# Optimization experiments

Measured on AMD Instinct MI355X. Metric: run time of the kernel, lower is better.

The kernel has to match this reference:

```python
import jax, jax.numpy as jnp
import numpy as np

HEADS = 4
NEG_SLOPE = 0.2  # PyG GATConv default


def gat_layer(x, src, dst, W, a_src, a_dst, b):
    """PyG-style GATConv: gather -> per-edge attention -> segment softmax -> scatter.
    x: [N, Fin], W: [Fin, H*C], a_src/a_dst: [H, C], b: [H*C]."""
    N = x.shape[0]
    h = (x @ W).reshape(N, HEADS, -1)                      # [N, H, C]
    alpha_s = jnp.einsum('nhc,hc->nh', h, a_src)           # [N, H]
    alpha_d = jnp.einsum('nhc,hc->nh', h, a_dst)           # [N, H]
    e = jax.nn.leaky_relu(alpha_s[src] + alpha_d[dst], NEG_SLOPE)  # [E, H]
    # segment softmax over incoming edges of each destination node
    m = jax.ops.segment_max(e, dst, num_segments=N)
    m = jnp.where(jnp.isfinite(m), m, 0.0)
    ex = jnp.exp(e - m[dst])
    denom = jax.ops.segment_sum(ex, dst, num_segments=N)
    alpha = ex / (denom[dst] + 1e-16)                      # [E, H]
    msg = h[src] * alpha[:, :, None]                       # [E, H, C]
    out = jax.ops.segment_sum(msg, dst, num_segments=N)    # [N, H, C]
    return out.reshape(N, -1) + b


def setup_inputs() -> dict:
    key = jax.random.key(0)
    ks = jax.random.split(key, 10)
    N, E, FIN, HID, OUT = 50000, 800000, 128, 128, 128
    hd1, hd2 = HID // HEADS, OUT // HEADS
    x = jax.random.normal(ks[0], (N, FIN), dtype=jnp.float32)
    edge_index = jax.random.randint(ks[1], (2, E), 0, N, dtype=jnp.int32)
    s1 = 1.0 / np.sqrt(FIN)
    s2 = 1.0 / np.sqrt(HID)
    return {
        'x_sub': x,
        'edge_index_sub': edge_index,
        'W1': jax.random.normal(ks[2], (FIN, HEADS * hd1), dtype=jnp.float32) * s1,
        'a_src1': jax.random.normal(ks[3], (HEADS, hd1), dtype=jnp.float32) * 0.1,
        'a_dst1': jax.random.normal(ks[4], (HEADS, hd1), dtype=jnp.float32) * 0.1,
        'b1': jnp.zeros((HEADS * hd1,), dtype=jnp.float32),
        'W2': jax.random.normal(ks[5], (HID, HEADS * hd2), dtype=jnp.float32) * s2,
        'a_src2': jax.random.normal(ks[6], (HEADS, hd2), dtype=jnp.float32) * 0.1,
        'a_dst2': jax.random.normal(ks[7], (HEADS, hd2), dtype=jnp.float32) * 0.1,
        'b2': jnp.zeros((HEADS * hd2,), dtype=jnp.float32),
    }


def reference(x_sub, edge_index_sub, W1, a_src1, a_dst1, b1, W2, a_src2, a_dst2, b2):
    N = x_sub.shape[0]
    # PyG GATConv default add_self_loops=True
    loops = jnp.arange(N, dtype=edge_index_sub.dtype)
    src = jnp.concatenate([edge_index_sub[0], loops])
    dst = jnp.concatenate([edge_index_sub[1], loops])
    h = gat_layer(x_sub, src, dst, W1, a_src1, a_dst1, b1)
    h = jax.nn.relu(h)  # dropout p=0.5 is identity in eval mode
    out = gat_layer(h, src, dst, W2, a_src2, a_dst2, b2)
    return out
```

## Files before the change

kernel.cpp:

```cpp
#include <hip/hip_runtime.h>
#include <hip/hip_fp16.h>

#define HEADS 4
#define F 128
#define NEG_SLOPE 0.2f

#define NB 256
#define NPB 196
#define BE 8192
#define CAPS 6144

#define LDP 136

typedef _Float16 f16x8 __attribute__((ext_vector_type(8)));
typedef _Float16 f16x4 __attribute__((ext_vector_type(4)));
typedef float f32x4 __attribute__((ext_vector_type(4)));

__device__ __forceinline__ float lrelu(float v) { return v > 0.f ? v : NEG_SLOPE * v; }

__global__ __launch_bounds__(256) void k_wcvt_hist(const float* __restrict__ W1,
                                                   const float* __restrict__ W2,
                                                   _Float16* __restrict__ Wt1,
                                                   _Float16* __restrict__ Wt2,
                                                   const int* __restrict__ dst,
                                                   int* __restrict__ histSlots,
                                                   int E, int gB) {
    __shared__ _Float16 l[128][LDP];
    __shared__ int hh[NB];
    int t = threadIdx.x;
    int bx = blockIdx.x;
    if (bx >= gB) {
        const float* W = (bx - gB) ? W2 : W1;
        _Float16* Wt = (bx - gB) ? Wt2 : Wt1;
        for (int i = t; i < 4096; i += 256) {
            int k = i >> 5, n4 = (i & 31) << 2;
            float4 v = ((const float4*)W)[i];
            l[n4][k]     = (_Float16)v.x;
            l[n4 + 1][k] = (_Float16)v.y;
            l[n4 + 2][k] = (_Float16)v.z;
            l[n4 + 3][k] = (_Float16)v.w;
        }
        __syncthreads();
        for (int i = t; i < 2048; i += 256) {
            int n = i >> 4, c8 = (i & 15) << 3;
            *(f16x8*)(Wt + n * 128 + c8) = *(const f16x8*)(&l[n][c8]);
        }
        return;
    }
    hh[t] = 0;
    __syncthreads();
    int base = bx * BE;
    int end = min(base + BE, E);
    for (int i = base + t; i < end; i += 256) atomicAdd(&hh[dst[i] / NPB], 1);
    __syncthreads();
    histSlots[bx * NB + t] = hh[t];
}

template <bool FP32IN>
__global__ __launch_bounds__(256) void k_gemm_mfma(const void* __restrict__ Xv,
                                                   const _Float16* __restrict__ Wt,
                                                   const float* __restrict__ asrc,
                                                   const float* __restrict__ adst,
                                                   _Float16* __restrict__ Hh,
                                                   float* __restrict__ As,
                                                   float* __restrict__ Ad, int N) {
    __shared__ _Float16 xs[64 * LDP];
    __shared__ _Float16 ws[128 * LDP];
    int t = threadIdx.x;
    int row0 = blockIdx.x * 64;

    for (int i = t; i < 128 * 16; i += 256) {
        int rw = i >> 4, c8 = (i & 15) << 3;
        *(f16x8*)(ws + rw * LDP + c8) = *(const f16x8*)(Wt + rw * 128 + c8);
    }
    if (FP32IN) {
        const float* Xf = (const float*)Xv;
        for (int i = t; i < 64 * 32; i += 256) {
            int r = i >> 5, c4 = (i & 31) << 2;
            int gr = row0 + r;
            float4 v = (gr < N) ? *(const float4*)(Xf + (size_t)gr * F + c4)
                                : make_float4(0.f, 0.f, 0.f, 0.f);
            f16x4 h4 = {(_Float16)v.x, (_Float16)v.y, (_Float16)v.z, (_Float16)v.w};
            *(f16x4*)(xs + r * LDP + c4) = h4;
        }
    } else {
        const _Float16* Xh = (const _Float16*)Xv;
        for (int i = t; i < 64 * 16; i += 256) {
            int r = i >> 4, c8 = (i & 15) << 3;
            int gr = row0 + r;
            f16x8 v = {0, 0, 0, 0, 0, 0, 0, 0};
            if (gr < N) v = *(const f16x8*)(Xh + (size_t)gr * F + c8);
            *(f16x8*)(xs + r * LDP + c8) = v;
        }
    }
    __syncthreads();

    int w = t >> 6, lane = t & 63, q = lane >> 4, r = lane & 15;
    f32x4 acc[8] = {};
    const _Float16* xrow = xs + (w * 16 + r) * LDP;
    const _Float16* wrow = ws + r * LDP;
#pragma unroll
    for (int kk = 0; kk < 4; ++kk) {
        f16x8 bx = *(const f16x8*)(xrow + kk * 32 + q * 8);
#pragma unroll
        for (int nt = 0; nt < 8; ++nt) {
            f16x8 af = *(const f16x8*)(wrow + nt * 16 * LDP + kk * 32 + q * 8);
            acc[nt] = __builtin_amdgcn_mfma_f32_16x16x32_f16(af, bx, acc[nt], 0, 0, 0);
        }
    }
    int m = row0 + w * 16 + r;

    float sh[4], dh[4];
#pragma unroll
    for (int h = 0; h < 4; ++h) {
        float s = 0.f, d = 0.f;
#pragma unroll
        for (int k2 = 0; k2 < 2; ++k2) {
            int nt = h * 2 + k2;
            float4 av = ((const float4*)asrc)[nt * 4 + q];
            float4 bv = ((const float4*)adst)[nt * 4 + q];
            s += acc[nt][0] * av.x + acc[nt][1] * av.y + acc[nt][2] * av.z + acc[nt][3] * av.w;
            d += acc[nt][0] * bv.x + acc[nt][1] * bv.y + acc[nt][2] * bv.z + acc[nt][3] * bv.w;
        }
        s += __shfl_xor(s, 16); s += __shfl_xor(s, 32);
        d += __shfl_xor(d, 16); d += __shfl_xor(d, 32);
        sh[h] = s; dh[h] = d;
    }
    if (q == 0 && m < N) {
        ((float4*)As)[m] = make_float4(sh[0], sh[1], sh[2], sh[3]);
        ((float4*)Ad)[m] = make_float4(dh[0], dh[1], dh[2], dh[3]);
    }
    if (m < N) {
        _Float16* hp = Hh + (size_t)m * F + q * 4;
#pragma unroll
        for (int nt = 0; nt < 8; ++nt) {
            f16x4 h4 = {(_Float16)acc[nt][0], (_Float16)acc[nt][1],
                        (_Float16)acc[nt][2], (_Float16)acc[nt][3]};
            *(f16x4*)(hp + nt * 16) = h4;
        }
    }
}

__global__ __launch_bounds__(NB) void k_bscan(const int* __restrict__ histSlots, int gB,
                                              int* __restrict__ bucketCnt,
                                              int* __restrict__ edgeStart,
                                              int* __restrict__ srcStart,
                                              int* __restrict__ bucketCursor,
                                              int* __restrict__ rowstart, int N) {
    __shared__ int ws1[4], ws2[4];
    int t = threadIdx.x, lane = t & 63, w = t >> 6;
    int c = 0;
    for (int i = 0; i < gB; ++i) c += histSlots[i * NB + t];
    bucketCnt[t] = c;
    int nIn = N - t * NPB; nIn = nIn < 0 ? 0 : (nIn > NPB ? NPB : nIn);
    int s = c + nIn;
    int x1 = c, x2 = s;
#pragma unroll
    for (int off = 1; off < 64; off <<= 1) {
        int a = __shfl_up(x1, off), b = __shfl_up(x2, off);
        if (lane >= off) { x1 += a; x2 += b; }
    }
    if (lane == 63) { ws1[w] = x1; ws2[w] = x2; }
    __syncthreads();
    int o1 = 0, o2 = 0;
    for (int i = 0; i < w; ++i) { o1 += ws1[i]; o2 += ws2[i]; }
    int e1 = o1 + x1 - c;
    int e2 = o2 + x2 - s;
    edgeStart[t] = e1; srcStart[t] = e2; bucketCursor[t] = e1;
    if (t == NB - 1) {
        edgeStart[NB] = e1 + c;
        srcStart[NB] = e2 + s;
        rowstart[N] = e2 + s;
    }
}

__global__ __launch_bounds__(256) void k_bscatter(const int* __restrict__ src,
                                                  const int* __restrict__ dst,
                                                  int* __restrict__ bucketCursor,
                                                  uint2* __restrict__ temp, int E) {
    __shared__ uint2 se[BE];
    __shared__ int hist[NB], lofs[NB], lcur[NB], gbase[NB];
    __shared__ int wsum[4];
    int t = threadIdx.x;
    hist[t] = 0;
    __syncthreads();
    int base = blockIdx.x * BE;
    int end = min(base + BE, E);
    for (int i = base + t; i < end; i += 256) atomicAdd(&hist[dst[i] / NPB], 1);
    __syncthreads();
    {
        int lane = t & 63, w = t >> 6;
        int c = hist[t], x = c;
#pragma unroll
        for (int off = 1; off < 64; off <<= 1) {
            int a = __shfl_up(x, off);
            if (lane >= off) x += a;
        }
        if (lane == 63) wsum[w] = x;
        __syncthreads();
        int o = 0;
        for (int i = 0; i < w; ++i) o += wsum[i];
        int ex = o + x - c;
        lofs[t] = ex;
        lcur[t] = ex;
        gbase[t] = c ? atomicAdd(&bucketCursor[t], c) : 0;
    }
    __syncthreads();
    for (int i = base + t; i < end; i += 256) {
        int d = dst[i];
        int b = d / NPB;
        int dl = d - b * NPB;
        int pos = atomicAdd(&lcur[b], 1);
        se[pos] = make_uint2((unsigned)src[i], (unsigned)((b << 8) | dl));
    }
    __syncthreads();
    int tot = end - base;
    for (int i = t; i < tot; i += 256) {
        uint2 e = se[i];
        int b = (int)(e.y >> 8);
        temp[gbase[b] + (i - lofs[b])] = e;
    }
}

__global__ __launch_bounds__(256) void k_bsort(const uint2* __restrict__ temp,
                                               const int* __restrict__ edgeStart,
                                               const int* __restrict__ srcStart,
                                               const int* __restrict__ bucketCnt,
                                               int* __restrict__ rowstart,
                                               int* __restrict__ srcs, int N) {
    __shared__ int cnt[NPB];
    __shared__ int scanE[NPB];
    __shared__ int outS[CAPS];
    __shared__ int wsum[4];
    int b = blockIdx.x, t = threadIdx.x;
    int eBase = edgeStart[b], eCnt = bucketCnt[b];
    int sBase = srcStart[b];
    int nIn = N - b * NPB; nIn = nIn < 0 ? 0 : (nIn > NPB ? NPB : nIn);
    for (int i = t; i < NPB; i += 256) cnt[i] = 1;
    __syncthreads();
    for (int i = t; i < eCnt; i += 256) {
        uint2 e = temp[eBase + i];
        atomicAdd(&cnt[e.y & 0xFF], 1);
    }
    __syncthreads();
    {
        int lane = t & 63, w = t >> 6;
        int c = (t < nIn) ? cnt[t] : 0;
        int x = c;
#pragma unroll
        for (int off = 1; off < 64; off <<= 1) {
            int a = __shfl_up(x, off);
            if (lane >= off) x += a;
        }
        if (lane == 63) wsum[w] = x;
        __syncthreads();
        int o = 0;
        for (int i = 0; i < w; ++i) o += wsum[i];
        if (t < nIn) scanE[t] = o + x - c;
    }
    __syncthreads();
    if (t < nIn) {
        int s0 = scanE[t];
        outS[s0] = b * NPB + t;
        cnt[t] = s0 + 1;
        rowstart[b * NPB + t] = sBase + s0;
    }
    __syncthreads();
    for (int i = t; i < eCnt; i += 256) {
        uint2 e = temp[eBase + i];
        int pos = atomicAdd(&cnt[e.y & 0xFF], 1);
        if (pos < CAPS) outS[pos] = (int)e.x;
    }
    __syncthreads();
    int tot = eCnt + nIn;
    for (int i = t; i < tot; i += 256) srcs[sBase + i] = outS[i];
}

template <bool RELU, bool OUTH>
__global__ __launch_bounds__(256) void k_aggr(const int* __restrict__ rowstart,
                                              const int* __restrict__ srcs,
                                              const float* __restrict__ As,
                                              const float* __restrict__ Ad,
                                              const _Float16* __restrict__ Hh,
                                              const float* __restrict__ bias,
                                              void* __restrict__ Ov, int N) {
    __shared__ float exs_s[4][256];
    int wid = threadIdx.x >> 6;
    float* exs = exs_s[wid];
    int w = (blockIdx.x << 2) + wid;
    int lane = threadIdx.x & 63;
    if (w >= N) return;
    int d = w;
    int b0 = rowstart[d], b1 = rowstart[d + 1];
    int g = lane >> 4, l16 = lane & 15;
    int h = l16 >> 2;
    float4 ad4 = ((const float4*)Ad)[d];
    float den = 0.f;
    float acc[8] = {};

    for (int base = b0; base < b1; base += 64) {
        int cnt = min(64, b1 - base);
        int myv = (lane < cnt) ? srcs[base + lane] : 0;
        if (lane < cnt) {
            float4 a4 = ((const float4*)As)[myv];
            float4 e;
            e.x = __expf(lrelu(a4.x + ad4.x));
            e.y = __expf(lrelu(a4.y + ad4.y));
            e.z = __expf(lrelu(a4.z + ad4.z));
            e.w = __expf(lrelu(a4.w + ad4.w));
            ((float4*)exs)[lane] = e;
        }
        int j = 0;
        for (; j + 8 <= cnt; j += 8) {
            int s0 = __shfl(myv, j + g);
            int s1 = __shfl(myv, j + 4 + g);
            float4 q0 = *(const float4*)(Hh + (size_t)s0 * F + 8 * l16);
            float4 q1 = *(const float4*)(Hh + (size_t)s1 * F + 8 * l16);
            float e0 = exs[(j + g) * 4 + h];
            float e1 = exs[(j + 4 + g) * 4 + h];
            den += e0 + e1;
            const __half2* p0 = (const __half2*)&q0;
            const __half2* p1 = (const __half2*)&q1;
#pragma unroll
            for (int u = 0; u < 4; ++u) {
                float2 f0 = __half22float2(p0[u]);
                float2 f1 = __half22float2(p1[u]);
                acc[2 * u]     += e0 * f0.x + e1 * f1.x;
                acc[2 * u + 1] += e0 * f0.y + e1 * f1.y;
            }
        }
        for (; j < cnt; j += 4) {
            int idx = j + g;
            bool ok = idx < cnt;
            int idxc = ok ? idx : (cnt - 1);
            int s0 = __shfl(myv, idxc);
            float e0 = ok ? exs[idx * 4 + h] : 0.f;
            float4 q0 = *(const float4*)(Hh + (size_t)s0 * F + 8 * l16);
            den += e0;
            const __half2* p0 = (const __half2*)&q0;
#pragma unroll
            for (int u = 0; u < 4; ++u) {
                float2 f0 = __half22float2(p0[u]);
                acc[2 * u]     += e0 * f0.x;
                acc[2 * u + 1] += e0 * f0.y;
            }
        }
    }
#pragma unroll
    for (int i = 0; i < 8; ++i) {
        acc[i] += __shfl_xor(acc[i], 16);
        acc[i] += __shfl_xor(acc[i], 32);
    }
    den += __shfl_xor(den, 16);
    den += __shfl_xor(den, 32);
    float inv = 1.f / (den + 1e-16f);

    if (g == 0) {
        float4 bv0 = ((const float4*)bias)[2 * l16];
        float4 bv1 = ((const float4*)bias)[2 * l16 + 1];
        float o[8];
        o[0] = acc[0] * inv + bv0.x; o[1] = acc[1] * inv + bv0.y;
        o[2] = acc[2] * inv + bv0.z; o[3] = acc[3] * inv + bv0.w;
        o[4] = acc[4] * inv + bv1.x; o[5] = acc[5] * inv + bv1.y;
        o[6] = acc[6] * inv + bv1.z; o[7] = acc[7] * inv + bv1.w;
        if (RELU) {
#pragma unroll
            for (int i = 0; i < 8; ++i) o[i] = fmaxf(o[i], 0.f);
        }
        if (OUTH) {
            f16x8 p;
#pragma unroll
            for (int i = 0; i < 8; ++i) p[i] = (_Float16)o[i];
            *(f16x8*)((_Float16*)Ov + (size_t)d * F + 8 * l16) = p;
        } else {
            float* op = (float*)Ov + (size_t)d * F + 8 * l16;
            *(float4*)op = make_float4(o[0], o[1], o[2], o[3]);
            *(float4*)(op + 4) = make_float4(o[4], o[5], o[6], o[7]);
        }
    }
}

extern "C" void kernel_launch(void* const* d_in, const int* in_sizes, int n_in,
                              void* d_out, int out_size, void* d_ws, size_t ws_size,
                              hipStream_t stream) {
    const float* x   = (const float*)d_in[0];
    const int*   ei  = (const int*)d_in[1];
    const float* W1  = (const float*)d_in[2];
    const float* as1 = (const float*)d_in[3];
    const float* ad1 = (const float*)d_in[4];
    const float* b1  = (const float*)d_in[5];
    const float* W2  = (const float*)d_in[6];
    const float* as2 = (const float*)d_in[7];
    const float* ad2 = (const float*)d_in[8];
    const float* b2  = (const float*)d_in[9];

    int N = in_sizes[0] / F;
    int E = in_sizes[1] / 2;
    const int* src = ei;
    const int* dst = ei + E;

    int gB = (E + BE - 1) / BE;

    char* base = (char*)d_ws;
    size_t off = 0;
    _Float16* Hh  = (_Float16*)(base + off); off += (size_t)N * F * 2;
    _Float16* O1h = (_Float16*)(base + off); off += (size_t)N * F * 2;
    float* As  = (float*)(base + off);  off += (size_t)N * HEADS * 4;
    float* Ad  = (float*)(base + off);  off += (size_t)N * HEADS * 4;
    int* rowstart = (int*)(base + off); off += (size_t)(N + 1) * 4;
    off = (off + 15) & ~(size_t)15;
    int* srcs = (int*)(base + off);     off += (size_t)(E + N) * 4;
    off = (off + 15) & ~(size_t)15;
    uint2* temp = (uint2*)(base + off); off += (size_t)E * 8;
    int* bucketCnt   = (int*)(base + off); off += NB * 4;
    int* edgeStart   = (int*)(base + off); off += (NB + 1) * 4;
    int* srcStart    = (int*)(base + off); off += (NB + 1) * 4;
    int* bucketCursor= (int*)(base + off); off += NB * 4;
    off = (off + 15) & ~(size_t)15;
    _Float16* Wt1 = (_Float16*)(base + off); off += 128 * 128 * 2;
    _Float16* Wt2 = (_Float16*)(base + off); off += 128 * 128 * 2;
    off = (off + 15) & ~(size_t)15;
    int* histSlots = (int*)(base + off); off += (size_t)gB * NB * 4;

    dim3 blk(256);
    int gG = (N + 63) / 64;
    int gW = (N + 3) / 4;

    k_wcvt_hist<<<gB + 2, blk, 0, stream>>>(W1, W2, Wt1, Wt2, dst, histSlots, E, gB);
    k_bscan<<<1, NB, 0, stream>>>(histSlots, gB, bucketCnt, edgeStart, srcStart,
                                  bucketCursor, rowstart, N);
    k_bscatter<<<gB, blk, 0, stream>>>(src, dst, bucketCursor, temp, E);
    k_bsort<<<NB, blk, 0, stream>>>(temp, edgeStart, srcStart, bucketCnt, rowstart, srcs, N);

    k_gemm_mfma<true><<<gG, blk, 0, stream>>>(x, Wt1, as1, ad1, Hh, As, Ad, N);
    k_aggr<true, true><<<gW, blk, 0, stream>>>(rowstart, srcs, As, Ad, Hh, b1, O1h, N);

    k_gemm_mfma<false><<<gG, blk, 0, stream>>>(O1h, Wt2, as2, ad2, Hh, As, Ad, N);
    k_aggr<false, false><<<gW, blk, 0, stream>>>(rowstart, srcs, As, Ad, Hh, b2, d_out, N);
}
```

Baseline: 170.3 us.

## Fuse edge bucket-scatter with layer-1 GEMM in one heterogeneous launch

Merges the edge bucket-scatter kernel and the layer-1 MFMA GEMM into a single launch, using block index ranges to pick the role, so the two independent stages run concurrently and one launch is removed. Shared memory becomes one union buffer, and the scatter chunk size is reduced so both roles fit in the same allocation. Smaller chunks mean more scatter blocks, more histogram slots, and more global cursor atomics. The layer-2 GEMM becomes a non-templated fp16-input kernel.

Measured after the change: 158.7 us. 6.8% less time.

```diff
diff --git a/kernel.cpp b/kernel.cpp
--- a/kernel.cpp
+++ b/kernel.cpp
@@ -7,10 +7,11 @@
 
 #define NB 256
 #define NPB 196
-#define BE 8192
+#define BE 5888
 #define CAPS 6144
 
 #define LDP 136
+#define SMEM_BYTES 52224
 
 typedef _Float16 f16x8 __attribute__((ext_vector_type(8)));
 typedef _Float16 f16x4 __attribute__((ext_vector_type(4)));
@@ -56,91 +57,6 @@
     histSlots[bx * NB + t] = hh[t];
 }
 
-template <bool FP32IN>
-__global__ __launch_bounds__(256) void k_gemm_mfma(const void* __restrict__ Xv,
-                                                   const _Float16* __restrict__ Wt,
-                                                   const float* __restrict__ asrc,
-                                                   const float* __restrict__ adst,
-                                                   _Float16* __restrict__ Hh,
-                                                   float* __restrict__ As,
-                                                   float* __restrict__ Ad, int N) {
-    __shared__ _Float16 xs[64 * LDP];
-    __shared__ _Float16 ws[128 * LDP];
-    int t = threadIdx.x;
-    int row0 = blockIdx.x * 64;
-
-    for (int i = t; i < 128 * 16; i += 256) {
-        int rw = i >> 4, c8 = (i & 15) << 3;
-        *(f16x8*)(ws + rw * LDP + c8) = *(const f16x8*)(Wt + rw * 128 + c8);
-    }
-    if (FP32IN) {
-        const float* Xf = (const float*)Xv;
-        for (int i = t; i < 64 * 32; i += 256) {
-            int r = i >> 5, c4 = (i & 31) << 2;
-            int gr = row0 + r;
-            float4 v = (gr < N) ? *(const float4*)(Xf + (size_t)gr * F + c4)
-                                : make_float4(0.f, 0.f, 0.f, 0.f);
-            f16x4 h4 = {(_Float16)v.x, (_Float16)v.y, (_Float16)v.z, (_Float16)v.w};
-            *(f16x4*)(xs + r * LDP + c4) = h4;
-        }
-    } else {
-        const _Float16* Xh = (const _Float16*)Xv;
-        for (int i = t; i < 64 * 16; i += 256) {
-            int r = i >> 4, c8 = (i & 15) << 3;
-            int gr = row0 + r;
-            f16x8 v = {0, 0, 0, 0, 0, 0, 0, 0};
-            if (gr < N) v = *(const f16x8*)(Xh + (size_t)gr * F + c8);
-            *(f16x8*)(xs + r * LDP + c8) = v;
-        }
-    }
-    __syncthreads();
-
-    int w = t >> 6, lane = t & 63, q = lane >> 4, r = lane & 15;
-    f32x4 acc[8] = {};
-    const _Float16* xrow = xs + (w * 16 + r) * LDP;
-    const _Float16* wrow = ws + r * LDP;
-#pragma unroll
-    for (int kk = 0; kk < 4; ++kk) {
-        f16x8 bx = *(const f16x8*)(xrow + kk * 32 + q * 8);
-#pragma unroll
-        for (int nt = 0; nt < 8; ++nt) {
-            f16x8 af = *(const f16x8*)(wrow + nt * 16 * LDP + kk * 32 + q * 8);
-            acc[nt] = __builtin_amdgcn_mfma_f32_16x16x32_f16(af, bx, acc[nt], 0, 0, 0);
-        }
-    }
-    int m = row0 + w * 16 + r;
-
-    float sh[4], dh[4];
-#pragma unroll
-    for (int h = 0; h < 4; ++h) {
-        float s = 0.f, d = 0.f;
-#pragma unroll
-        for (int k2 = 0; k2 < 2; ++k2) {
-            int nt = h * 2 + k2;
-            float4 av = ((const float4*)asrc)[nt * 4 + q];
-            float4 bv = ((const float4*)adst)[nt * 4 + q];
-            s += acc[nt][0] * av.x + acc[nt][1] * av.y + acc[nt][2] * av.z + acc[nt][3] * av.w;
-            d += acc[nt][0] * bv.x + acc[nt][1] * bv.y + acc[nt][2] * bv.z + acc[nt][3] * bv.w;
-        }
-        s += __shfl_xor(s, 16); s += __shfl_xor(s, 32);
-        d += __shfl_xor(d, 16); d += __shfl_xor(d, 32);
-        sh[h] = s; dh[h] = d;
-    }
-    if (q == 0 && m < N) {
-        ((float4*)As)[m] = make_float4(sh[0], sh[1], sh[2], sh[3]);
-        ((float4*)Ad)[m] = make_float4(dh[0], dh[1], dh[2], dh[3]);
-    }
-    if (m < N) {
-        _Float16* hp = Hh + (size_t)m * F + q * 4;
-#pragma unroll
-        for (int nt = 0; nt < 8; ++nt) {
-            f16x4 h4 = {(_Float16)acc[nt][0], (_Float16)acc[nt][1],
-                        (_Float16)acc[nt][2], (_Float16)acc[nt][3]};
-            *(f16x4*)(hp + nt * 16) = h4;
-        }
-    }
-}
-
 __global__ __launch_bounds__(NB) void k_bscan(const int* __restrict__ histSlots, int gB,
                                               int* __restrict__ bucketCnt,
                                               int* __restrict__ edgeStart,
@@ -174,51 +90,201 @@
     }
 }
 
-__global__ __launch_bounds__(256) void k_bscatter(const int* __restrict__ src,
-                                                  const int* __restrict__ dst,
-                                                  int* __restrict__ bucketCursor,
-                                                  uint2* __restrict__ temp, int E) {
-    __shared__ uint2 se[BE];
-    __shared__ int hist[NB], lofs[NB], lcur[NB], gbase[NB];
-    __shared__ int wsum[4];
+__global__ __launch_bounds__(256) void k_scat_gemm(const int* __restrict__ src,
+                                                   const int* __restrict__ dst,
+                                                   int* __restrict__ bucketCursor,
+                                                   uint2* __restrict__ temp, int E, int gB,
+                                                   const float* __restrict__ X,
+                                                   const _Float16* __restrict__ Wt,
+                                                   const float* __restrict__ asrc,
+                                                   const float* __restrict__ adst,
+                                                   _Float16* __restrict__ Hh,
+                                                   float* __restrict__ As,
+                                                   float* __restrict__ Ad, int N) {
+    __shared__ __align__(16) char smem[SMEM_BYTES];
     int t = threadIdx.x;
-    hist[t] = 0;
-    __syncthreads();
-    int base = blockIdx.x * BE;
-    int end = min(base + BE, E);
-    for (int i = base + t; i < end; i += 256) atomicAdd(&hist[dst[i] / NPB], 1);
-    __syncthreads();
-    {
-        int lane = t & 63, w = t >> 6;
-        int c = hist[t], x = c;
-#pragma unroll
-        for (int off = 1; off < 64; off <<= 1) {
-            int a = __shfl_up(x, off);
-            if (lane >= off) x += a;
-        }
-        if (lane == 63) wsum[w] = x;
+    int bx = blockIdx.x;
+
+    if (bx < gB) {
+        uint2* se   = (uint2*)smem;
+        int* hist   = (int*)(smem + BE * 8);
+        int* lofs   = hist + NB;
+        int* lcur   = lofs + NB;
+        int* gbase  = lcur + NB;
+        int* wsum   = gbase + NB;
+        hist[t] = 0;
         __syncthreads();
-        int o = 0;
-        for (int i = 0; i < w; ++i) o += wsum[i];
-        int ex = o + x - c;
-        lofs[t] = ex;
-        lcur[t] = ex;
-        gbase[t] = c ? atomicAdd(&bucketCursor[t], c) : 0;
-    }
-    __syncthreads();
-    for (int i = base + t; i < end; i += 256) {
-        int d = dst[i];
-        int b = d / NPB;
-        int dl = d - b * NPB;
-        int pos = atomicAdd(&lcur[b], 1);
-        se[pos] = make_uint2((unsigned)src[i], (unsigned)((b << 8) | dl));
-    }
-    __syncthreads();
-    int tot = end - base;
-    for (int i = t; i < tot; i += 256) {
-        uint2 e = se[i];
-        int b = (int)(e.y >> 8);
-        temp[gbase[b] + (i - lofs[b])] = e;
+        int base = bx * BE;
+        int end = min(base + BE, E);
+        for (int i = base + t; i < end; i += 256) atomicAdd(&hist[dst[i] / NPB], 1);
+        __syncthreads();
+        {
+            int lane = t & 63, w = t >> 6;
+            int c = hist[t], x = c;
+#pragma unroll
+            for (int off = 1; off < 64; off <<= 1) {
+                int a = __shfl_up(x, off);
+                if (lane >= off) x += a;
+            }
+            if (lane == 63) wsum[w] = x;
+            __syncthreads();
+            int o = 0;
+            for (int i = 0; i < w; ++i) o += wsum[i];
+            int ex = o + x - c;
+            lofs[t] = ex;
+            lcur[t] = ex;
+            gbase[t] = c ? atomicAdd(&bucketCursor[t], c) : 0;
+        }
+        __syncthreads();
+        for (int i = base + t; i < end; i += 256) {
+            int d = dst[i];
+            int b = d / NPB;
+            int dl = d - b * NPB;
+            int pos = atomicAdd(&lcur[b], 1);
+            se[pos] = make_uint2((unsigned)src[i], (unsigned)((b << 8) | dl));
+        }
+        __syncthreads();
+        int tot = end - base;
+        for (int i = t; i < tot; i += 256) {
+            uint2 e = se[i];
+            int b = (int)(e.y >> 8);
+            temp[gbase[b] + (i - lofs[b])] = e;
+        }
+        return;
+    }
+
+    _Float16* xs = (_Float16*)smem;
+    _Float16* ws = xs + 64 * LDP;
+    int row0 = (bx - gB) * 64;
+
+    for (int i = t; i < 128 * 16; i += 256) {
+        int rw = i >> 4, c8 = (i & 15) << 3;
+        *(f16x8*)(ws + rw * LDP + c8) = *(const f16x8*)(Wt + rw * 128 + c8);
+    }
+    for (int i = t; i < 64 * 32; i += 256) {
+        int r = i >> 5, c4 = (i & 31) << 2;
+        int gr = row0 + r;
+        float4 v = (gr < N) ? *(const float4*)(X + (size_t)gr * F + c4)
+                            : make_float4(0.f, 0.f, 0.f, 0.f);
+        f16x4 h4 = {(_Float16)v.x, (_Float16)v.y, (_Float16)v.z, (_Float16)v.w};
+        *(f16x4*)(xs + r * LDP + c4) = h4;
+    }
+    __syncthreads();
+
+    int w = t >> 6, lane = t & 63, q = lane >> 4, r = lane & 15;
+    f32x4 acc[8] = {};
+    const _Float16* xrow = xs + (w * 16 + r) * LDP;
+    const _Float16* wrow = ws + r * LDP;
+#pragma unroll
+    for (int kk = 0; kk < 4; ++kk) {
+        f16x8 bxv = *(const f16x8*)(xrow + kk * 32 + q * 8);
+#pragma unroll
+        for (int nt = 0; nt < 8; ++nt) {
+            f16x8 af = *(const f16x8*)(wrow + nt * 16 * LDP + kk * 32 + q * 8);
+            acc[nt] = __builtin_amdgcn_mfma_f32_16x16x32_f16(af, bxv, acc[nt], 0, 0, 0);
+        }
+    }
+    int m = row0 + w * 16 + r;
+
+    float sh[4], dh[4];
+#pragma unroll
+    for (int h = 0; h < 4; ++h) {
+        float s = 0.f, d = 0.f;
+#pragma unroll
+        for (int k2 = 0; k2 < 2; ++k2) {
+            int nt = h * 2 + k2;
+            float4 av = ((const float4*)asrc)[nt * 4 + q];
+            float4 bv = ((const float4*)adst)[nt * 4 + q];
+            s += acc[nt][0] * av.x + acc[nt][1] * av.y + acc[nt][2] * av.z + acc[nt][3] * av.w;
+            d += acc[nt][0] * bv.x + acc[nt][1] * bv.y + acc[nt][2] * bv.z + acc[nt][3] * bv.w;
+        }
+        s += __shfl_xor(s, 16); s += __shfl_xor(s, 32);
+        d += __shfl_xor(d, 16); d += __shfl_xor(d, 32);
+        sh[h] = s; dh[h] = d;
+    }
+    if (q == 0 && m < N) {
+        ((float4*)As)[m] = make_float4(sh[0], sh[1], sh[2], sh[3]);
+        ((float4*)Ad)[m] = make_float4(dh[0], dh[1], dh[2], dh[3]);
+    }
+    if (m < N) {
+        _Float16* hp = Hh + (size_t)m * F + q * 4;
+#pragma unroll
+        for (int nt = 0; nt < 8; ++nt) {
+            f16x4 h4 = {(_Float16)acc[nt][0], (_Float16)acc[nt][1],
+                        (_Float16)acc[nt][2], (_Float16)acc[nt][3]};
+            *(f16x4*)(hp + nt * 16) = h4;
+        }
+    }
+}
+
+__global__ __launch_bounds__(256) void k_gemm_mfma(const _Float16* __restrict__ Xh,
+                                                   const _Float16* __restrict__ Wt,
+                                                   const float* __restrict__ asrc,
+                                                   const float* __restrict__ adst,
+                                                   _Float16* __restrict__ Hh,
+                                                   float* __restrict__ As,
+                                                   float* __restrict__ Ad, int N) {
+    __shared__ _Float16 xs[64 * LDP];
+    __shared__ _Float16 ws[128 * LDP];
+    int t = threadIdx.x;
+    int row0 = blockIdx.x * 64;
+
+    for (int i = t; i < 128 * 16; i += 256) {
+        int rw = i >> 4, c8 = (i & 15) << 3;
+        *(f16x8*)(ws + rw * LDP + c8) = *(const f16x8*)(Wt + rw * 128 + c8);
+    }
+    for (int i = t; i < 64 * 16; i += 256) {
+        int r = i >> 4, c8 = (i & 15) << 3;
+        int gr = row0 + r;
+        f16x8 v = {0, 0, 0, 0, 0, 0, 0, 0};
+        if (gr < N) v = *(const f16x8*)(Xh + (size_t)gr * F + c8);
+        *(f16x8*)(xs + r * LDP + c8) = v;
+    }
+    __syncthreads();
+
+    int w = t >> 6, lane = t & 63, q = lane >> 4, r = lane & 15;
+    f32x4 acc[8] = {};
+    const _Float16* xrow = xs + (w * 16 + r) * LDP;
+    const _Float16* wrow = ws + r * LDP;
+#pragma unroll
+    for (int kk = 0; kk < 4; ++kk) {
+        f16x8 bxv = *(const f16x8*)(xrow + kk * 32 + q * 8);
+#pragma unroll
+        for (int nt = 0; nt < 8; ++nt) {
+            f16x8 af = *(const f16x8*)(wrow + nt * 16 * LDP + kk * 32 + q * 8);
+            acc[nt] = __builtin_amdgcn_mfma_f32_16x16x32_f16(af, bxv, acc[nt], 0, 0, 0);
+        }
+    }
+    int m = row0 + w * 16 + r;
+
+    float sh[4], dh[4];
+#pragma unroll
+    for (int h = 0; h < 4; ++h) {
+        float s = 0.f, d = 0.f;
+#pragma unroll
+        for (int k2 = 0; k2 < 2; ++k2) {
+            int nt = h * 2 + k2;
+            float4 av = ((const float4*)asrc)[nt * 4 + q];
+            float4 bv = ((const float4*)adst)[nt * 4 + q];
+            s += acc[nt][0] * av.x + acc[nt][1] * av.y + acc[nt][2] * av.z + acc[nt][3] * av.w;
+            d += acc[nt][0] * bv.x + acc[nt][1] * bv.y + acc[nt][2] * bv.z + acc[nt][3] * bv.w;
+        }
+        s += __shfl_xor(s, 16); s += __shfl_xor(s, 32);
+        d += __shfl_xor(d, 16); d += __shfl_xor(d, 32);
+        sh[h] = s; dh[h] = d;
+    }
+    if (q == 0 && m < N) {
+        ((float4*)As)[m] = make_float4(sh[0], sh[1], sh[2], sh[3]);
+        ((float4*)Ad)[m] = make_float4(dh[0], dh[1], dh[2], dh[3]);
+    }
+    if (m < N) {
+        _Float16* hp = Hh + (size_t)m * F + q * 4;
+#pragma unroll
+        for (int nt = 0; nt < 8; ++nt) {
+            f16x4 h4 = {(_Float16)acc[nt][0], (_Float16)acc[nt][1],
+                        (_Float16)acc[nt][2], (_Float16)acc[nt][3]};
+            *(f16x4*)(hp + nt * 16) = h4;
+        }
     }
 }
 
@@ -400,6 +466,8 @@
     const int* dst = ei + E;
 
     int gB = (E + BE - 1) / BE;
+    int gG = (N + 63) / 64;
+    int gW = (N + 3) / 4;
 
     char* base = (char*)d_ws;
     size_t off = 0;
@@ -423,18 +491,16 @@
     int* histSlots = (int*)(base + off); off += (size_t)gB * NB * 4;
 
     dim3 blk(256);
-    int gG = (N + 63) / 64;
-    int gW = (N + 3) / 4;
 
     k_wcvt_hist<<<gB + 2, blk, 0, stream>>>(W1, W2, Wt1, Wt2, dst, histSlots, E, gB);
     k_bscan<<<1, NB, 0, stream>>>(histSlots, gB, bucketCnt, edgeStart, srcStart,
                                   bucketCursor, rowstart, N);
-    k_bscatter<<<gB, blk, 0, stream>>>(src, dst, bucketCursor, temp, E);
+    k_scat_gemm<<<gB + gG, blk, 0, stream>>>(src, dst, bucketCursor, temp, E, gB,
+                                             x, Wt1, as1, ad1, Hh, As, Ad, N);
     k_bsort<<<NB, blk, 0, stream>>>(temp, edgeStart, srcStart, bucketCnt, rowstart, srcs, N);
 
-    k_gemm_mfma<true><<<gG, blk, 0, stream>>>(x, Wt1, as1, ad1, Hh, As, Ad, N);
     k_aggr<true, true><<<gW, blk, 0, stream>>>(rowstart, srcs, As, Ad, Hh, b1, O1h, N);
 
-    k_gemm_mfma<false><<<gG, blk, 0, stream>>>(O1h, Wt2, as2, ad2, Hh, As, Ad, N);
+    k_gemm_mfma<<<gG, blk, 0, stream>>>(O1h, Wt2, as2, ad2, Hh, As, Ad, N);
     k_aggr<false, false><<<gW, blk, 0, stream>>>(rowstart, srcs, As, Ad, Hh, b2, d_out, N);
 }
```
